# Kernel optimization log

Hardware: AMD Instinct MI355X
Metric: run time of the kernel (lower is better)

Reference implementation:

```python
import jax, jax.numpy as jnp
import numpy as np
import math

FACTOR = 5  # Informer 'factor' hyperparameter


def setup_inputs() -> dict:
    key = jax.random.key(0)
    B, L, H, D = 2, 2048, 16, 128
    k1, k2, k3, k4 = jax.random.split(key, 4)
    queries = jax.random.normal(k1, (B, L, H, D), jnp.float32)
    keys = jax.random.normal(k2, (B, L, H, D), jnp.float32)
    values = jax.random.normal(k3, (B, L, H, D), jnp.float32)
    sample_k = max(1, min(FACTOR * math.ceil(math.log(L)), L))  # u in the paper
    index_sample = jax.random.randint(k4, (L, sample_k), 0, L, dtype=jnp.int32)
    return {"queries": queries, "keys": keys, "values": values,
            "index_sample": index_sample}


def reference(queries, keys, values, index_sample):
    # queries/keys/values: [B, L, H, D] -> [B, H, L, D]
    Q = jnp.swapaxes(queries, 1, 2)
    K = jnp.swapaxes(keys, 1, 2)
    V = jnp.swapaxes(values, 1, 2)
    B, H, L_Q, D = Q.shape
    L_K = K.shape[2]
    # U_part = factor*ceil(ln L_K), clipped to L_K then to L_Q (n_top in _prob_QK)
    n_top = max(1, min(FACTOR * math.ceil(math.log(L_K)), L_K, L_Q))

    # --- _prob_QK: sampled scores ---
    # K_sample: [B, H, L_Q, sample_k, D] (same materialization as torch K_expand gather)
    K_sample = K[:, :, index_sample, :]
    Q_K_sample = jnp.einsum('bhqd,bhqsd->bhqs', Q, K_sample)
    # sparsity measure M: max - mean(over full L_K, per original torch code)
    M = Q_K_sample.max(axis=-1) - Q_K_sample.sum(axis=-1) / L_K  # [B,H,L_Q]
    _, M_top = jax.lax.top_k(M, n_top)  # [B,H,n_top]

    # gather top queries and compute their full attention rows
    Q_reduce = jnp.take_along_axis(Q, M_top[..., None], axis=2)  # [B,H,u,D]
    scores = jnp.einsum('bhud,bhkd->bhuk', Q_reduce, K)  # [B,H,u,L_K]
    scale = 1.0 / math.sqrt(D)
    scores = scores * scale

    # --- initial context (mask_flag=False): mean of V over keys ---
    context = jnp.broadcast_to(V.mean(axis=2, keepdims=True), (B, H, L_Q, D))

    # --- update context at top-query positions ---
    attn = jax.nn.softmax(scores, axis=-1)
    upd = jnp.einsum('bhuk,bhkd->bhud', attn, V)  # [B,H,u,D]
    bi = jnp.arange(B)[:, None, None]
    hi = jnp.arange(H)[None, :, None]
    context = context.at[bi, hi, M_top].set(upd)

    return jnp.swapaxes(context, 1, 2)  # [B, L_Q, H, D]
```

## Files before the change

### kernel.cpp

```cpp
#include <hip/hip_runtime.h>
#include <math.h>

#define B_    2
#define L_    2048
#define H_    16
#define D_    128
#define S_    40
#define NTOP_ 40
#define NCH_  8
#define CHK_  256
#define VCH_  32
#define CAND_ 512

#define SCALE_ 0.08838834764831843f

typedef _Float16 half2_t __attribute__((ext_vector_type(2)));

__device__ __forceinline__ half2_t as_h2(unsigned int u) {
    union { unsigned int u; half2_t h; } x; x.u = u; return x.h;
}
__device__ __forceinline__ unsigned int h2pack(float a, float b) {
    union { half2_t h; unsigned int u; } x;
    x.h[0] = (_Float16)a; x.h[1] = (_Float16)b; return x.u;
}
#if __has_builtin(__builtin_amdgcn_fdot2)
__device__ __forceinline__ float FDOT2(half2_t a, half2_t b, float c) {
    return __builtin_amdgcn_fdot2(a, b, c, false);
}
#else
__device__ __forceinline__ float FDOT2(half2_t a, half2_t b, float c) {
    return c + (float)a[0] * (float)b[0] + (float)a[1] * (float)b[1];
}
#endif

__device__ __forceinline__ unsigned int encf(float f) {
    unsigned int u = __float_as_uint(f);
    return (u & 0x80000000u) ? ~u : (u | 0x80000000u);
}
__device__ __forceinline__ float decf(unsigned int e) {
    unsigned int u = (e & 0x80000000u) ? (e ^ 0x80000000u) : ~e;
    return __uint_as_float(u);
}

__global__ __launch_bounds__(256) void kA_pack_vpart(const float* __restrict__ K,
                                                     const float* __restrict__ V,
                                                     unsigned int* __restrict__ Kf,
                                                     float* __restrict__ vpart,
                                                     int npack) {
    const int bid = blockIdx.x, t = threadIdx.x;
    if (bid < npack) {
        const int bh = bid >> 3, kc = bid & 7;
        const int h = bh & 15, b = bh >> 4;
        const float4* K4 = (const float4*)K;
        uint2* out2 = (uint2*)Kf;
        for (int j = 0; j < 32; ++j) {
            const int g = j * 256 + t;
            const int row = g >> 5, c = g & 31;
            const float4 v = K4[((size_t)(b * L_ + kc * 256 + row) * H_ + h) * 32 + c];
            out2[(size_t)(bh * L_ + kc * 256 + row) * 32 + c] =
                make_uint2(h2pack(v.x, v.y), h2pack(v.z, v.w));
        }
    } else {
        __shared__ float red[256];
        const int vbid = bid - npack;
        const int bh  = vbid >> 5;
        const int lc  = vbid & (VCH_ - 1);
        const int h   = bh & 15, b = bh >> 4;
        const int d   = t & (D_ - 1);
        const int sub = t >> 7;
        float acc = 0.0f;
        const int l0 = lc * (L_ / VCH_);
        for (int l = l0 + sub; l < l0 + L_ / VCH_; l += 2)
            acc += V[((size_t)(b * L_ + l) * H_ + h) * D_ + d];
        red[t] = acc;
        __syncthreads();
        if (t < D_) vpart[(size_t)vbid * D_ + t] = red[t] + red[t + 128];
    }
}

__global__ __launch_bounds__(256) void k1_sample_f16(const float* __restrict__ Q,
                                                     const uint4* __restrict__ KF,
                                                     const int* __restrict__ idx,
                                                     float* __restrict__ M) {
    const int sb   = blockIdx.x;
    const int xcd  = sb & 7;
    const int li   = sb >> 3;
    const int bh   = (xcd << 2) + (li >> 9);
    const int rb   = li & 511;
    const int t    = threadIdx.x;
    const int wave = t >> 6, lane = t & 63;
    const int q    = rb * 4 + wave;
    const int h    = bh & 15, b = bh >> 4;
    const int g    = lane >> 3, sub = lane & 7;

    const float4* Q4 = (const float4*)Q;
    const size_t rowQ = ((size_t)(b * L_ + q) * H_ + h) * 32;
    const int* ip = idx + q * S_;
    int kidx[5];
    #pragma unroll
    for (int s = 0; s < 5; ++s) kidx[s] = ip[s * 8 + g];

    const float4 qa0 = Q4[rowQ + 2 * sub];
    const float4 qa1 = Q4[rowQ + 2 * sub + 1];
    const float4 qb0 = Q4[rowQ + 16 + 2 * sub];
    const float4 qb1 = Q4[rowQ + 16 + 2 * sub + 1];

    uint4 kv[5][2];
    #pragma unroll
    for (int s = 0; s < 5; ++s) {
        const uint4* kr = KF + ((size_t)bh * L_ + kidx[s]) * 16;
        kv[s][0] = kr[sub];
        kv[s][1] = kr[8 + sub];
    }
    __builtin_amdgcn_sched_barrier(0);

    half2_t qh[8];
    qh[0][0] = (_Float16)qa0.x; qh[0][1] = (_Float16)qa0.y;
    qh[1][0] = (_Float16)qa0.z; qh[1][1] = (_Float16)qa0.w;
    qh[2][0] = (_Float16)qa1.x; qh[2][1] = (_Float16)qa1.y;
    qh[3][0] = (_Float16)qa1.z; qh[3][1] = (_Float16)qa1.w;
    qh[4][0] = (_Float16)qb0.x; qh[4][1] = (_Float16)qb0.y;
    qh[5][0] = (_Float16)qb0.z; qh[5][1] = (_Float16)qb0.w;
    qh[6][0] = (_Float16)qb1.x; qh[6][1] = (_Float16)qb1.y;
    qh[7][0] = (_Float16)qb1.z; qh[7][1] = (_Float16)qb1.w;

    float smax = -INFINITY, ssum = 0.0f;
    #pragma unroll
    for (int s = 0; s < 5; ++s) {
        float p = 0.f;
        p = FDOT2(qh[0], as_h2(kv[s][0].x), p);
        p = FDOT2(qh[1], as_h2(kv[s][0].y), p);
        p = FDOT2(qh[2], as_h2(kv[s][0].z), p);
        p = FDOT2(qh[3], as_h2(kv[s][0].w), p);
        p = FDOT2(qh[4], as_h2(kv[s][1].x), p);
        p = FDOT2(qh[5], as_h2(kv[s][1].y), p);
        p = FDOT2(qh[6], as_h2(kv[s][1].z), p);
        p = FDOT2(qh[7], as_h2(kv[s][1].w), p);
        p += __shfl_xor(p, 1);
        p += __shfl_xor(p, 2);
        p += __shfl_xor(p, 4);
        smax = fmaxf(smax, p);
        ssum += p;
    }
    #pragma unroll
    for (int o = 8; o < 64; o <<= 1) {
        smax = fmaxf(smax, __shfl_xor(smax, o));
        ssum += __shfl_xor(ssum, o);
    }
    if (lane == 0) M[(size_t)bh * L_ + q] = smax - ssum * (1.0f / L_);
}

__global__ __launch_bounds__(256) void k1_sample_f32(const float* __restrict__ Q,
                                                     const float* __restrict__ K,
                                                     const int* __restrict__ idx,
                                                     float* __restrict__ M) {
    const int sb   = blockIdx.x;
    const int xcd  = sb & 7;
    const int li   = sb >> 3;
    const int bh   = (xcd << 2) + (li >> 9);
    const int rb   = li & 511;
    const int t    = threadIdx.x;
    const int wave = t >> 6, lane = t & 63;
    const int q    = rb * 4 + wave;
    const int h    = bh & 15, b = bh >> 4;
    const int g    = lane >> 3, sub = lane & 7;

    const float4* Q4 = (const float4*)Q;
    const float4* K4 = (const float4*)K;
    const size_t rowQ = ((size_t)(b * L_ + q) * H_ + h) * 32;
    const size_t kbase = ((size_t)b * L_ * H_ + h) * 32 + sub;
    const int* ip = idx + q * S_;
    int kidx[5];
    #pragma unroll
    for (int s = 0; s < 5; ++s) kidx[s] = ip[s * 8 + g];
    const float4 qv0 = Q4[rowQ + 0 + sub];
    const float4 qv1 = Q4[rowQ + 8 + sub];
    const float4 qv2 = Q4[rowQ + 16 + sub];
    const float4 qv3 = Q4[rowQ + 24 + sub];
    float4 kv[5][4];
    #pragma unroll
    for (int s = 0; s < 5; ++s) {
        const float4* kb = K4 + kbase + (size_t)kidx[s] * (H_ * 32);
        kv[s][0] = kb[0]; kv[s][1] = kb[8]; kv[s][2] = kb[16]; kv[s][3] = kb[24];
    }
    __builtin_amdgcn_sched_barrier(0);
    float smax = -INFINITY, ssum = 0.0f;
    #pragma unroll
    for (int s = 0; s < 5; ++s) {
        float p = qv0.x * kv[s][0].x + qv0.y * kv[s][0].y + qv0.z * kv[s][0].z + qv0.w * kv[s][0].w
                + qv1.x * kv[s][1].x + qv1.y * kv[s][1].y + qv1.z * kv[s][1].z + qv1.w * kv[s][1].w
                + qv2.x * kv[s][2].x + qv2.y * kv[s][2].y + qv2.z * kv[s][2].z + qv2.w * kv[s][2].w
                + qv3.x * kv[s][3].x + qv3.y * kv[s][3].y + qv3.z * kv[s][3].z + qv3.w * kv[s][3].w;
        p += __shfl_xor(p, 1);
        p += __shfl_xor(p, 2);
        p += __shfl_xor(p, 4);
        smax = fmaxf(smax, p);
        ssum += p;
    }
    #pragma unroll
    for (int o = 8; o < 64; o <<= 1) {
        smax = fmaxf(smax, __shfl_xor(smax, o));
        ssum += __shfl_xor(ssum, o);
    }
    if (lane == 0) M[(size_t)bh * L_ + q] = smax - ssum * (1.0f / L_);
}

__global__ __launch_bounds__(1024) void k2_rank_refine(const float* __restrict__ Mws,
                                                       const float* __restrict__ Q,
                                                       const float* __restrict__ K,
                                                       const int* __restrict__ idx,
                                                       const float* __restrict__ vpart,
                                                       float* __restrict__ vmean,
                                                       int* __restrict__ topk,
                                                       float delta) {
    const int bid = blockIdx.x, t = threadIdx.x;
    if (bid == 32) {
        for (int e = t; e < 32 * D_; e += 1024) {
            const int bh = e >> 7, d = e & 127;
            float s = 0.f;
            #pragma unroll
            for (int c = 0; c < VCH_; ++c)
                s += vpart[(size_t)(bh * VCH_ + c) * D_ + d];
            vmean[e] = s * (1.0f / L_);
        }
        return;
    }
    __shared__ unsigned int ue[L_];
    __shared__ int hist[256], sscan[256];
    __shared__ int sh_chosen, sh_need, sh_nc;
    __shared__ int clist[CAND_];
    __shared__ float cMx[CAND_];
    __shared__ unsigned int cmaxe[CAND_];
    __shared__ float csum[CAND_];
    const int bh = bid, h = bh & 15, b = bh >> 4;
    const float* Mrow = Mws + (size_t)bh * L_;
    for (int i = t; i < L_; i += 1024) ue[i] = encf(Mrow[i]);
    if (t == 0) sh_nc = 0;
    __syncthreads();

    unsigned int prefix = 0; int need = NTOP_;
    for (int l = 3; l >= 0; --l) {
        if (t < 256) hist[t] = 0;
        __syncthreads();
        for (int i = t; i < L_; i += 1024) {
            const unsigned int u = ue[i];
            const bool match = (l == 3) || ((u >> (8 * (l + 1))) == prefix);
            if (match) atomicAdd(&hist[(u >> (8 * l)) & 255], 1);
        }
        __syncthreads();
        if (t < 256) sscan[t] = hist[t];
        __syncthreads();
        for (int off = 1; off < 256; off <<= 1) {
            int v = 0;
            if (t < 256 && t + off < 256) v = sscan[t + off];
            __syncthreads();
            if (t < 256) sscan[t] += v;
            __syncthreads();
        }
        if (t < 256) {
            const int above = sscan[t] - hist[t];
            if (above < need && need <= above + hist[t]) { sh_chosen = t; sh_need = need - above; }
        }
        __syncthreads();
        prefix = (prefix << 8) | (unsigned int)sh_chosen;
        need = sh_need;
        __syncthreads();
    }
    const unsigned int ethr = encf(decf(prefix) - delta);
    for (int i = t; i < L_; i += 1024) {
        if (ue[i] >= ethr) {
            const int p = atomicAdd(&sh_nc, 1);
            if (p < CAND_) clist[p] = i;
        }
    }
    __syncthreads();
    const int nc = min(sh_nc, CAND_);
    for (int i = t; i < CAND_; i += 1024) { cmaxe[i] = 0x007FFFFFu; csum[i] = 0.f; }
    __syncthreads();

    const float4* Q4 = (const float4*)Q;
    const float4* K4 = (const float4*)K;
    const int grp = t >> 3, sub = t & 7;
    for (int task = grp; task < nc * S_; task += 128) {
        const int ci = task / S_;
        const int s  = task - ci * S_;
        const int qq = clist[ci];
        const int ki = idx[qq * S_ + s];
        const float4* Kr = K4 + ((size_t)(b * L_ + ki) * H_ + h) * 32;
        const float4* Qr = Q4 + ((size_t)(b * L_ + qq) * H_ + h) * 32;
        float p = 0.f;
        #pragma unroll
        for (int qt2 = 0; qt2 < 4; ++qt2) {
            const float4 kv = Kr[qt2 * 8 + sub];
            const float4 qv = Qr[qt2 * 8 + sub];
            p += qv.x * kv.x + qv.y * kv.y + qv.z * kv.z + qv.w * kv.w;
        }
        p += __shfl_xor(p, 1);
        p += __shfl_xor(p, 2);
        p += __shfl_xor(p, 4);
        if (sub == 0) {
            atomicMax(&cmaxe[ci], encf(p));
            atomicAdd(&csum[ci], p);
        }
    }
    __syncthreads();
    if (t < nc) cMx[t] = decf(cmaxe[t]) - csum[t] * (1.0f / L_);
    __syncthreads();
    if (t < nc) {
        const float mi = cMx[t]; const int qi = clist[t];
        int rk = 0;
        for (int j = 0; j < nc; ++j) {
            const float mj = cMx[j];
            rk += (mj > mi) || (mj == mi && clist[j] < qi);
        }
        if (rk < NTOP_) topk[bh * NTOP_ + rk] = qi;
    }
}

__global__ __launch_bounds__(256) void k3_scorepv_fill(const float* __restrict__ Q,
                                                       const float* __restrict__ K,
                                                       const float* __restrict__ V,
                                                       const int* __restrict__ topk,
                                                       const float* __restrict__ vmean,
                                                       float* __restrict__ pmax,
                                                       float* __restrict__ psum,
                                                       float* __restrict__ pout,
                                                       float* __restrict__ out) {
    __shared__ float Qs[10 * 132];
    __shared__ float S[10 * 260];
    __shared__ float mrow[10];
    __shared__ int   tq[10];
    const int bid0 = blockIdx.x;
    const int t   = threadIdx.x;

    if (bid0 >= 1024) {
        const int fb = bid0 - 1024;
        const float4* vm4 = (const float4*)vmean;
        float4* out4 = (float4*)out;
        const size_t base = (size_t)fb * 4096;
        #pragma unroll
        for (int k = 0; k < 16; ++k) {
            const size_t i = base + k * 256 + t;
            const int d4 = (int)(i & 31);
            const int h  = (int)((i >> 5) & 15);
            const int b  = (int)(i >> 20);
            out4[i] = vm4[((b << 4) + h) * 32 + d4];
        }
        return;
    }

    const int xcd = bid0 & 7;
    const int loc = bid0 >> 3;
    const int bh  = (xcd << 2) + (loc >> 5);
    const int rem = loc & 31;
    const int kc  = rem >> 2;
    const int uq4 = rem & 3;
    const int h   = bh & 15, b = bh >> 4;

    if (t < 10) tq[t] = topk[bh * NTOP_ + uq4 * 10 + t];
    __syncthreads();

    {
        const float4* Q4 = (const float4*)Q;
        #pragma unroll
        for (int it = 0; it < 2; ++it) {
            const int i = it * 256 + t;
            if (i < 320) {
                const int u = i >> 5, dc = i & 31;
                *(float4*)&Qs[u * 132 + dc * 4] =
                    Q4[((size_t)(b * L_ + tq[u]) * H_ + h) * 32 + dc];
            }
        }
    }
    __syncthreads();

    {
        const int kq2 = t >> 1, ug = t & 1;
        float acc[2][5];
        #pragma unroll
        for (int j = 0; j < 2; ++j)
            #pragma unroll
            for (int uu = 0; uu < 5; ++uu) acc[j][uu] = 0.f;
        const float4* Kb = (const float4*)K +
            ((size_t)(b * L_ + kc * CHK_ + kq2 * 2) * H_ + h) * 32;
        for (int dc = 0; dc < 32; ++dc) {
            float4 qv[5];
            #pragma unroll
            for (int uu = 0; uu < 5; ++uu)
                qv[uu] = *(const float4*)&Qs[(ug * 5 + uu) * 132 + dc * 4];
            #pragma unroll
            for (int j = 0; j < 2; ++j) {
                const float4 kv = Kb[(size_t)j * (H_ * 32) + dc];
                #pragma unroll
                for (int uu = 0; uu < 5; ++uu)
                    acc[j][uu] += qv[uu].x * kv.x + qv[uu].y * kv.y
                                + qv[uu].z * kv.z + qv[uu].w * kv.w;
            }
        }
        #pragma unroll
        for (int j = 0; j < 2; ++j)
            #pragma unroll
            for (int uu = 0; uu < 5; ++uu)
                S[(ug * 5 + uu) * 260 + kq2 * 2 + j] = acc[j][uu] * SCALE_;
    }
    __syncthreads();

    {
        const int w = t >> 6, lane = t & 63;
        #pragma unroll
        for (int uu = 0; uu < 3; ++uu) {
            const int u = w + 4 * uu;
            if (u < 10) {
                const float* Sr = S + u * 260;
                float v = fmaxf(fmaxf(Sr[lane], Sr[lane + 64]),
                                fmaxf(Sr[lane + 128], Sr[lane + 192]));
                #pragma unroll
                for (int o = 1; o < 64; o <<= 1) v = fmaxf(v, __shfl_xor(v, o, 64));
                if (lane == 0) mrow[u] = v;
            }
        }
    }
    __syncthreads();

    for (int e = t; e < 10 * 256; e += 256) {
        const int u = e >> 8, k = e & 255;
        S[u * 260 + k] = __expf(S[u * 260 + k] - mrow[u]);
    }
    __syncthreads();

    {
        const int w = t >> 6, lane = t & 63;
        #pragma unroll
        for (int uu = 0; uu < 3; ++uu) {
            const int u = w + 4 * uu;
            if (u < 10) {
                const float* Sr = S + u * 260;
                float v = Sr[lane] + Sr[lane + 64] + Sr[lane + 128] + Sr[lane + 192];
                #pragma unroll
                for (int o = 1; o < 64; o <<= 1) v += __shfl_xor(v, o, 64);
                if (lane == 0) {
                    psum[(bh * NCH_ + kc) * NTOP_ + uq4 * 10 + u] = v;
                    pmax[(bh * NCH_ + kc) * NTOP_ + uq4 * 10 + u] = mrow[u];
                }
            }
        }
    }

    {
        const int g = t >> 6, d2 = t & 63;
        float accA[3], accB[3];
        #pragma unroll
        for (int uu = 0; uu < 3; ++uu) { accA[uu] = 0.f; accB[uu] = 0.f; }
        const float2* Vb = (const float2*)(V + ((size_t)(b * L_ + kc * CHK_) * H_ + h) * D_) + d2;
        for (int kq = 0; kq < CHK_ / 4; ++kq) {
            float2 v0 = Vb[(size_t)(kq * 4 + 0) * (H_ * D_ / 2)];
            float2 v1 = Vb[(size_t)(kq * 4 + 1) * (H_ * D_ / 2)];
            float2 v2 = Vb[(size_t)(kq * 4 + 2) * (H_ * D_ / 2)];
            float2 v3 = Vb[(size_t)(kq * 4 + 3) * (H_ * D_ / 2)];
            #pragma unroll
            for (int uu = 0; uu < 3; ++uu) {
                const int u = g + 4 * uu;
                if (u < 10) {
                    const float4 p = *(const float4*)&S[u * 260 + kq * 4];
                    accA[uu] += p.x * v0.x + p.y * v1.x + p.z * v2.x + p.w * v3.x;
                    accB[uu] += p.x * v0.y + p.y * v1.y + p.z * v2.y + p.w * v3.y;
                }
            }
        }
        #pragma unroll
        for (int uu = 0; uu < 3; ++uu) {
            const int u = g + 4 * uu;
            if (u < 10) {
                float* pb = pout + (((size_t)(bh * NCH_ + kc)) * NTOP_ + uq4 * 10 + u) * D_ + d2 * 2;
                *(float2*)pb = make_float2(accA[uu], accB[uu]);
            }
        }
    }
}

__global__ __launch_bounds__(128) void k_comb(const float* __restrict__ pmax,
                                              const float* __restrict__ psum,
                                              const float* __restrict__ pout,
                                              const int* __restrict__ topk,
                                              float* __restrict__ out) {
    const int bid = blockIdx.x;
    const int bh  = bid / NTOP_;
    const int u   = bid - bh * NTOP_;
    const int h   = bh & 15, b = bh >> 4;
    const int t   = threadIdx.x;

    float pm[NCH_];
    float M = -INFINITY;
    #pragma unroll
    for (int c = 0; c < NCH_; ++c) {
        pm[c] = pmax[(bh * NCH_ + c) * NTOP_ + u];
        M = fmaxf(M, pm[c]);
    }
    float ssum = 0.0f, o = 0.0f;
    #pragma unroll
    for (int c = 0; c < NCH_; ++c) {
        const float w = __expf(pm[c] - M);
        ssum += psum[(bh * NCH_ + c) * NTOP_ + u] * w;
        o += pout[((size_t)(bh * NCH_ + c) * NTOP_ + u) * D_ + t] * w;
    }
    const int qi = topk[bh * NTOP_ + u];
    out[((size_t)(b * L_ + qi) * H_ + h) * D_ + t] = o / ssum;
}

extern "C" void kernel_launch(void* const* d_in, const int* in_sizes, int n_in,
                              void* d_out, int out_size, void* d_ws, size_t ws_size,
                              hipStream_t stream) {
    const float* Q  = (const float*)d_in[0];
    const float* K  = (const float*)d_in[1];
    const float* V  = (const float*)d_in[2];
    const int* idx  = (const int*)d_in[3];
    float* out      = (float*)d_out;

    char* ws = (char*)d_ws;
    size_t off = 0;
    float* Mws   = (float*)(ws + off); off += (size_t)65536 * 4;
    float* vpart = (float*)(ws + off); off += (size_t)1024 * 128 * 4;
    float* vmean = (float*)(ws + off); off += (size_t)4096 * 4;
    int*   topk  = (int*)(ws + off);   off += 1280 * 4;
    float* pmax  = (float*)(ws + off); off += (size_t)256 * 40 * 4;
    float* psum  = (float*)(ws + off); off += (size_t)256 * 40 * 4;
    float* pout  = (float*)(ws + off); off += (size_t)256 * 40 * 128 * 4;
    unsigned int* Kf = (unsigned int*)(ws + off);
    const size_t kf_bytes = (size_t)32 * L_ * D_ * 2;
    const bool use_f16 = (ws_size >= off + kf_bytes);

    if (use_f16) {
        hipLaunchKernelGGL(kA_pack_vpart, dim3(256 + 1024), dim3(256), 0, stream,
                           K, V, Kf, vpart, 256);
        hipLaunchKernelGGL(k1_sample_f16, dim3(16384), dim3(256), 0, stream,
                           Q, (const uint4*)Kf, idx, Mws);
    } else {
        hipLaunchKernelGGL(kA_pack_vpart, dim3(1024), dim3(256), 0, stream,
                           K, V, Kf, vpart, 0);
        hipLaunchKernelGGL(k1_sample_f32, dim3(16384), dim3(256), 0, stream,
                           Q, K, idx, Mws);
    }
    hipLaunchKernelGGL(k2_rank_refine, dim3(33), dim3(1024), 0, stream,
                       Mws, Q, K, idx, vpart, vmean, topk, use_f16 ? 0.5f : 0.01f);
    hipLaunchKernelGGL(k3_scorepv_fill, dim3(1536), dim3(256), 0, stream,
                       Q, K, V, topk, vmean, pmax, psum, pout, out);
    hipLaunchKernelGGL(k_comb, dim3(1280), dim3(128), 0, stream,
                       pmax, psum, pout, topk, out);
}
```

Baseline: 151.5 us.

## Process all 40 top queries per block to reuse K/V chunk loads

Restructures the score+PV kernel so each 1024-thread block handles all 40 top queries for one (batch, head, key-chunk) instead of splitting queries into four blocks. K and V chunks are then loaded once per chunk rather than four times. The QK dot product now uses 16-lane shuffle reductions with Q held in registers, and the PV step splits keys across two wave groups, combining them through shared memory. The trade-off is fewer, larger blocks (384 vs 1536), more shared memory per block and extra shuffle work.

After: 153.0 us. About the same (+1.0%).

```diff
diff --git a/kernel.cpp b/kernel.cpp
--- a/kernel.cpp
+++ b/kernel.cpp
@@ -317,30 +317,30 @@
     }
 }
 
-__global__ __launch_bounds__(256) void k3_scorepv_fill(const float* __restrict__ Q,
-                                                       const float* __restrict__ K,
-                                                       const float* __restrict__ V,
-                                                       const int* __restrict__ topk,
-                                                       const float* __restrict__ vmean,
-                                                       float* __restrict__ pmax,
-                                                       float* __restrict__ psum,
-                                                       float* __restrict__ pout,
-                                                       float* __restrict__ out) {
-    __shared__ float Qs[10 * 132];
-    __shared__ float S[10 * 260];
-    __shared__ float mrow[10];
-    __shared__ int   tq[10];
+__global__ __launch_bounds__(1024) void k3_scorepv_fill(const float* __restrict__ Q,
+                                                        const float* __restrict__ K,
+                                                        const float* __restrict__ V,
+                                                        const int* __restrict__ topk,
+                                                        const float* __restrict__ vmean,
+                                                        float* __restrict__ pmax,
+                                                        float* __restrict__ psum,
+                                                        float* __restrict__ pout,
+                                                        float* __restrict__ out) {
+    __shared__ float S[40 * 260];
+    __shared__ float2 Ppv[40][64];
+    __shared__ float mrow[40];
+    __shared__ int   tq[40];
     const int bid0 = blockIdx.x;
     const int t   = threadIdx.x;
 
-    if (bid0 >= 1024) {
-        const int fb = bid0 - 1024;
+    if (bid0 >= 256) {
+        const int fb = bid0 - 256;
         const float4* vm4 = (const float4*)vmean;
         float4* out4 = (float4*)out;
-        const size_t base = (size_t)fb * 4096;
+        const size_t base = (size_t)fb * 16384;
         #pragma unroll
         for (int k = 0; k < 16; ++k) {
-            const size_t i = base + k * 256 + t;
+            const size_t i = base + k * 1024 + t;
             const int d4 = (int)(i & 31);
             const int h  = (int)((i >> 5) & 15);
             const int b  = (int)(i >> 20);
@@ -351,66 +351,58 @@
 
     const int xcd = bid0 & 7;
     const int loc = bid0 >> 3;
-    const int bh  = (xcd << 2) + (loc >> 5);
-    const int rem = loc & 31;
-    const int kc  = rem >> 2;
-    const int uq4 = rem & 3;
+    const int bh  = (xcd << 2) + (loc >> 3);
+    const int kc  = loc & 7;
     const int h   = bh & 15, b = bh >> 4;
-
-    if (t < 10) tq[t] = topk[bh * NTOP_ + uq4 * 10 + t];
+    const int w   = t >> 6, lane = t & 63;
+
+    if (t < 40) tq[t] = topk[bh * NTOP_ + t];
     __syncthreads();
 
     {
+        const int uq = w & 3, kr = w >> 2;
+        const int keysub = lane >> 4, slice = lane & 15;
         const float4* Q4 = (const float4*)Q;
+        const float4* K4 = (const float4*)K;
         #pragma unroll
-        for (int it = 0; it < 2; ++it) {
-            const int i = it * 256 + t;
-            if (i < 320) {
-                const int u = i >> 5, dc = i & 31;
-                *(float4*)&Qs[u * 132 + dc * 4] =
-                    Q4[((size_t)(b * L_ + tq[u]) * H_ + h) * 32 + dc];
+        for (int half = 0; half < 2; ++half) {
+            float4 qr0[5], qr1[5];
+            #pragma unroll
+            for (int u5 = 0; u5 < 5; ++u5) {
+                const int u = uq * 10 + half * 5 + u5;
+                const size_t qb = ((size_t)(b * L_ + tq[u]) * H_ + h) * 32 + slice * 2;
+                qr0[u5] = Q4[qb];
+                qr1[u5] = Q4[qb + 1];
             }
+            for (int it = 0; it < 16; ++it) {
+                const int key = kc * CHK_ + kr * 64 + it * 4 + keysub;
+                const float4* Kr = K4 + ((size_t)(b * L_ + key) * H_ + h) * 32 + slice * 2;
+                const float4 k0 = Kr[0];
+                const float4 k1v = Kr[1];
+                #pragma unroll
+                for (int u5 = 0; u5 < 5; ++u5) {
+                    float acc = qr0[u5].x * k0.x + qr0[u5].y * k0.y
+                              + qr0[u5].z * k0.z + qr0[u5].w * k0.w
+                              + qr1[u5].x * k1v.x + qr1[u5].y * k1v.y
+                              + qr1[u5].z * k1v.z + qr1[u5].w * k1v.w;
+                    acc += __shfl_xor(acc, 1);
+                    acc += __shfl_xor(acc, 2);
+                    acc += __shfl_xor(acc, 4);
+                    acc += __shfl_xor(acc, 8);
+                    if (slice == 0)
+                        S[(uq * 10 + half * 5 + u5) * 260 + kr * 64 + it * 4 + keysub] =
+                            acc * SCALE_;
+                }
+            }
         }
     }
     __syncthreads();
 
     {
-        const int kq2 = t >> 1, ug = t & 1;
-        float acc[2][5];
         #pragma unroll
-        for (int j = 0; j < 2; ++j)
-            #pragma unroll
-            for (int uu = 0; uu < 5; ++uu) acc[j][uu] = 0.f;
-        const float4* Kb = (const float4*)K +
-            ((size_t)(b * L_ + kc * CHK_ + kq2 * 2) * H_ + h) * 32;
-        for (int dc = 0; dc < 32; ++dc) {
-            float4 qv[5];
-            #pragma unroll
-            for (int uu = 0; uu < 5; ++uu)
-                qv[uu] = *(const float4*)&Qs[(ug * 5 + uu) * 132 + dc * 4];
-            #pragma unroll
-            for (int j = 0; j < 2; ++j) {
-                const float4 kv = Kb[(size_t)j * (H_ * 32) + dc];
-                #pragma unroll
-                for (int uu = 0; uu < 5; ++uu)
-                    acc[j][uu] += qv[uu].x * kv.x + qv[uu].y * kv.y
-                                + qv[uu].z * kv.z + qv[uu].w * kv.w;
-            }
-        }
-        #pragma unroll
-        for (int j = 0; j < 2; ++j)
-            #pragma unroll
-            for (int uu = 0; uu < 5; ++uu)
-                S[(ug * 5 + uu) * 260 + kq2 * 2 + j] = acc[j][uu] * SCALE_;
-    }
-    __syncthreads();
-
-    {
-        const int w = t >> 6, lane = t & 63;
-        #pragma unroll
-        for (int uu = 0; uu < 3; ++uu) {
-            const int u = w + 4 * uu;
-            if (u < 10) {
+        for (int j = 0; j < 3; ++j) {
+            const int u = w + 16 * j;
+            if (u < NTOP_) {
                 const float* Sr = S + u * 260;
                 float v = fmaxf(fmaxf(Sr[lane], Sr[lane + 64]),
                                 fmaxf(Sr[lane + 128], Sr[lane + 192]));
@@ -422,57 +414,61 @@
     }
     __syncthreads();
 
-    for (int e = t; e < 10 * 256; e += 256) {
+    for (int e = t; e < NTOP_ * 256; e += 1024) {
         const int u = e >> 8, k = e & 255;
         S[u * 260 + k] = __expf(S[u * 260 + k] - mrow[u]);
     }
     __syncthreads();
 
     {
-        const int w = t >> 6, lane = t & 63;
         #pragma unroll
-        for (int uu = 0; uu < 3; ++uu) {
-            const int u = w + 4 * uu;
-            if (u < 10) {
+        for (int j = 0; j < 3; ++j) {
+            const int u = w + 16 * j;
+            if (u < NTOP_) {
                 const float* Sr = S + u * 260;
                 float v = Sr[lane] + Sr[lane + 64] + Sr[lane + 128] + Sr[lane + 192];
                 #pragma unroll
                 for (int o = 1; o < 64; o <<= 1) v += __shfl_xor(v, o, 64);
                 if (lane == 0) {
-                    psum[(bh * NCH_ + kc) * NTOP_ + uq4 * 10 + u] = v;
-                    pmax[(bh * NCH_ + kc) * NTOP_ + uq4 * 10 + u] = mrow[u];
+                    psum[(bh * NCH_ + kc) * NTOP_ + u] = v;
+                    pmax[(bh * NCH_ + kc) * NTOP_ + u] = mrow[u];
                 }
             }
         }
     }
 
     {
-        const int g = t >> 6, d2 = t & 63;
-        float accA[3], accB[3];
+        const int kr2 = w & 1, ug = w >> 1;
+        const int d2 = lane;
+        float accA[5], accB[5];
         #pragma unroll
-        for (int uu = 0; uu < 3; ++uu) { accA[uu] = 0.f; accB[uu] = 0.f; }
-        const float2* Vb = (const float2*)(V + ((size_t)(b * L_ + kc * CHK_) * H_ + h) * D_) + d2;
-        for (int kq = 0; kq < CHK_ / 4; ++kq) {
-            float2 v0 = Vb[(size_t)(kq * 4 + 0) * (H_ * D_ / 2)];
-            float2 v1 = Vb[(size_t)(kq * 4 + 1) * (H_ * D_ / 2)];
-            float2 v2 = Vb[(size_t)(kq * 4 + 2) * (H_ * D_ / 2)];
-            float2 v3 = Vb[(size_t)(kq * 4 + 3) * (H_ * D_ / 2)];
+        for (int u5 = 0; u5 < 5; ++u5) { accA[u5] = 0.f; accB[u5] = 0.f; }
+        const float2* Vb = (const float2*)(V +
+            ((size_t)(b * L_ + kc * CHK_ + kr2 * 128) * H_ + h) * D_) + d2;
+        for (int kq = 0; kq < 32; ++kq) {
+            const float2 v0 = Vb[(size_t)(kq * 4 + 0) * (H_ * D_ / 2)];
+            const float2 v1 = Vb[(size_t)(kq * 4 + 1) * (H_ * D_ / 2)];
+            const float2 v2 = Vb[(size_t)(kq * 4 + 2) * (H_ * D_ / 2)];
+            const float2 v3 = Vb[(size_t)(kq * 4 + 3) * (H_ * D_ / 2)];
             #pragma unroll
-            for (int uu = 0; uu < 3; ++uu) {
-                const int u = g + 4 * uu;
-                if (u < 10) {
-                    const float4 p = *(const float4*)&S[u * 260 + kq * 4];
-                    accA[uu] += p.x * v0.x + p.y * v1.x + p.z * v2.x + p.w * v3.x;
-                    accB[uu] += p.x * v0.y + p.y * v1.y + p.z * v2.y + p.w * v3.y;
-                }
+            for (int u5 = 0; u5 < 5; ++u5) {
+                const float4 p = *(const float4*)&S[(ug * 5 + u5) * 260 + kr2 * 128 + kq * 4];
+                accA[u5] += p.x * v0.x + p.y * v1.x + p.z * v2.x + p.w * v3.x;
+                accB[u5] += p.x * v0.y + p.y * v1.y + p.z * v2.y + p.w * v3.y;
             }
         }
-        #pragma unroll
-        for (int uu = 0; uu < 3; ++uu) {
-            const int u = g + 4 * uu;
-            if (u < 10) {
-                float* pb = pout + (((size_t)(bh * NCH_ + kc)) * NTOP_ + uq4 * 10 + u) * D_ + d2 * 2;
-                *(float2*)pb = make_float2(accA[uu], accB[uu]);
+        if (kr2 == 1) {
+            #pragma unroll
+            for (int u5 = 0; u5 < 5; ++u5)
+                Ppv[ug * 5 + u5][d2] = make_float2(accA[u5], accB[u5]);
+        }
+        __syncthreads();
+        if (kr2 == 0) {
+            #pragma unroll
+            for (int u5 = 0; u5 < 5; ++u5) {
+                const float2 o = Ppv[ug * 5 + u5][d2];
+                float* pb = pout + (((size_t)(bh * NCH_ + kc)) * NTOP_ + ug * 5 + u5) * D_ + d2 * 2;
+                *(float2*)pb = make_float2(accA[u5] + o.x, accB[u5] + o.y);
             }
         }
     }
@@ -542,7 +538,7 @@
     }
     hipLaunchKernelGGL(k2_rank_refine, dim3(33), dim3(1024), 0, stream,
                        Mws, Q, K, idx, vpart, vmean, topk, use_f16 ? 0.5f : 0.01f);
-    hipLaunchKernelGGL(k3_scorepv_fill, dim3(1536), dim3(256), 0, stream,
+    hipLaunchKernelGGL(k3_scorepv_fill, dim3(384), dim3(1024), 0, stream,
                        Q, K, V, topk, vmean, pmax, psum, pout, out);
     hipLaunchKernelGGL(k_comb, dim3(1280), dim3(128), 0, stream,
                        pmax, psum, pout, topk, out);
```
